# Performance work log

Measured on AMD Instinct MI355X. Metric: run time of the kernel, lower is better.

The kernel has to match this reference:

```python
import jax, jax.numpy as jnp
import numpy as np

N = 50000        # nodes
E = 800000       # edges (before self-loops)
F_IN = 256       # input feature dim
HID = 64         # hidden per head (concat=False -> head mean)
NCLS = 40        # classes
HEADS = 8
NEG_SLOPE = 0.2  # PyG GATConv default leaky_relu slope


def setup_inputs() -> dict:
    key = jax.random.key(0)
    ks = jax.random.split(key, 11)
    s = 0.1
    return {
        "x": jax.random.normal(ks[0], (N, F_IN), jnp.float32),
        "edge_index": jax.random.randint(ks[1], (2, E), 0, N, dtype=jnp.int64),
        "edge_attr": jax.random.uniform(ks[2], (E, 1), jnp.float32),
        "W0": jax.random.normal(ks[3], (HEADS * HID, F_IN), jnp.float32) * s,
        "a0s": jax.random.normal(ks[4], (HEADS, HID), jnp.float32) * s,
        "a0d": jax.random.normal(ks[5], (HEADS, HID), jnp.float32) * s,
        "b0": jnp.zeros((HID,), jnp.float32),
        "W2": jax.random.normal(ks[6], (HEADS * NCLS, HID), jnp.float32) * s,
        "a2s": jax.random.normal(ks[7], (HEADS, NCLS), jnp.float32) * s,
        "a2d": jax.random.normal(ks[8], (HEADS, NCLS), jnp.float32) * s,
        "b2": jnp.zeros((NCLS,), jnp.float32),
    }


def _gat_conv(x, src, dst, W, att_src, att_dst, bias, heads, out_c):
    # Linear: [N, in] @ [heads*out, in]^T -> [N, heads, out]
    h = (x @ W.T).reshape(N, heads, out_c)
    # Per-node attention logits, gathered per edge.
    a_s = jnp.einsum('nhc,hc->nh', h, att_src)
    a_d = jnp.einsum('nhc,hc->nh', h, att_dst)
    e = jax.nn.leaky_relu(a_s[src] + a_d[dst], NEG_SLOPE)  # [E, H]
    # Segment softmax over incoming edges of each destination node.
    m = jax.ops.segment_max(e, dst, num_segments=N)
    p = jnp.exp(e - m[dst])
    denom = jax.ops.segment_sum(p, dst, num_segments=N)
    alpha = p / (denom[dst] + 1e-16)
    # Weighted message scatter-sum: [E,H,C] -> [N,H,C]
    out = jax.ops.segment_sum(alpha[:, :, None] * h[src], dst, num_segments=N)
    # concat=False -> mean over heads, then bias.
    return out.mean(axis=1) + bias


def reference(x, edge_index, edge_attr, W0, a0s, a0d, b0, W2, a2s, a2d, b2):
    # edge_attr is unpacked by the torch forward but never used by GATConv.
    # PyG GATConv adds self-loops by default.
    loops = jnp.arange(N, dtype=edge_index.dtype)
    src = jnp.concatenate([edge_index[0], loops])
    dst = jnp.concatenate([edge_index[1], loops])
    h = jax.nn.relu(_gat_conv(x, src, dst, W0, a0s, a0d, b0, HEADS, HID))
    # dropout is identity in eval mode
    out = _gat_conv(h, src, dst, W2, a2s, a2d, b2, HEADS, NCLS)
    return jax.nn.log_softmax(out, axis=1)
```

## Files before the change

### kernel.cpp

```cpp
#include <hip/hip_runtime.h>
#include <hip/hip_bf16.h>
#include <math.h>


#define NEG_SLOPE 0.2f

typedef short v8s __attribute__((ext_vector_type(8)));
typedef float v4f __attribute__((ext_vector_type(4)));
typedef float v2f __attribute__((ext_vector_type(2)));
typedef unsigned short u16;
typedef unsigned int u32;
typedef unsigned char u8;

__device__ __forceinline__ u16 f2bf(float f) {
    union { float f; u32 u; } v; v.f = f;
    u32 r = v.u + 0x7fffu + ((v.u >> 16) & 1u);
    return (u16)(r >> 16);
}
__device__ __forceinline__ float lrelu_exp(float e) {
    e = (e > 0.f) ? e : NEG_SLOPE * e;
    return __expf(e);
}
__device__ __forceinline__ void dec8(uint2 r, float* h) {
    v2f a = __builtin_amdgcn_cvt_pk_f32_fp8(r.x, false);
    v2f b = __builtin_amdgcn_cvt_pk_f32_fp8(r.x, true);
    v2f c = __builtin_amdgcn_cvt_pk_f32_fp8(r.y, false);
    v2f d = __builtin_amdgcn_cvt_pk_f32_fp8(r.y, true);
    h[0] = a.x; h[1] = a.y; h[2] = b.x; h[3] = b.y;
    h[4] = c.x; h[5] = c.y; h[6] = d.x; h[7] = d.y;
}
__device__ __forceinline__ u8 enc8(float v) {
    u32 p = __builtin_amdgcn_cvt_pk_fp8_f32(v, v, 0u, false);
    return (u8)(p & 0xffu);
}


__global__ __launch_bounds__(256) void histcast_k(const int* __restrict__ ei, int* __restrict__ deg,
                                                  int E, int Nn, int NBh,
                                                  const float* __restrict__ x, u16* __restrict__ xb,
                                                  const float* __restrict__ W0, u16* __restrict__ W0b,
                                                  const float* __restrict__ W2, u16* __restrict__ W2b,
                                                  int nx, int n0c, int n2c) {
    int b = blockIdx.x;
    if (b < NBh) {
        int e = b * 256 + threadIdx.x;
        int ET = E + Nn;
        if (e >= ET) return;
        int d = (e < E) ? ei[E + e] : (e - E);
        atomicAdd(&deg[d], 1);
    } else {
        int i = ((b - NBh) * 256 + threadIdx.x) * 4;
        const float* in; u16* out;
        if (i < nx)            { in = x;  out = xb; }
        else if (i < nx + n0c) { in = W0; out = W0b; i -= nx; }
        else if (i < nx + n0c + n2c) { in = W2; out = W2b; i -= nx + n0c; }
        else return;
        float4 v = *reinterpret_cast<const float4*>(in + i);
        ushort4 o;
        o.x = f2bf(v.x); o.y = f2bf(v.y); o.z = f2bf(v.z); o.w = f2bf(v.w);
        *reinterpret_cast<ushort4*>(out + i) = o;
    }
}


__global__ __launch_bounds__(1024) void scanA_k(const int* __restrict__ deg, int* __restrict__ incl,
                                                int* __restrict__ bsum, int n) {
    __shared__ int wsum[16];
    int t = threadIdx.x;
    int i = blockIdx.x * 1024 + t;
    int v = (i < n) ? deg[i] : 0;
    int lane = t & 63, wid = t >> 6;
    int sv = v;
    for (int off = 1; off < 64; off <<= 1) {
        int u = __shfl_up(sv, off, 64);
        if (lane >= off) sv += u;
    }
    if (lane == 63) wsum[wid] = sv;
    __syncthreads();
    if (t < 16) {
        int w = wsum[t];
        for (int off = 1; off < 16; off <<= 1) {
            int u = __shfl_up(w, off, 64);
            if (t >= off) w += u;
        }
        wsum[t] = w;
    }
    __syncthreads();
    int pre = (wid > 0) ? wsum[wid - 1] : 0;
    int inc = pre + sv;
    if (i < n) incl[i] = inc;
    if (t == 1023) bsum[blockIdx.x] = inc;
}


__global__ __launch_bounds__(256) void scanBC_k(const int* __restrict__ incl, const int* __restrict__ deg,
                                                const int* __restrict__ bsum, int* __restrict__ rowstart,
                                                int n, int B) {
    __shared__ int sb[65];
    int t = threadIdx.x;
    if (t < 64) {
        int v = (t < B) ? bsum[t] : 0;
        int sv = v;
        for (int off = 1; off < 64; off <<= 1) {
            int u = __shfl_up(sv, off, 64);
            if (t >= off) sv += u;
        }
        sb[t] = sv - v;
        if (t == 63) sb[64] = sv;
    }
    __syncthreads();
    int i = blockIdx.x * 256 + t;
    if (i < n) rowstart[i] = sb[i >> 10] + incl[i] - deg[i];
    if (i == 0) rowstart[n] = sb[64];
}

__global__ __launch_bounds__(256) void scatter_k(const int* __restrict__ ei,
                                                 const int* __restrict__ rowstart,
                                                 int* __restrict__ cursor,
                                                 int* __restrict__ srcs, int E, int Nn) {
    int e = blockIdx.x * 256 + threadIdx.x;
    int ET = E + Nn;
    if (e >= ET) return;
    int s, d;
    if (e < E) { s = ei[e]; d = ei[E + e]; }
    else       { s = e - E; d = e - E; }
    int pos = atomicAdd(&cursor[d], 1);
    srcs[rowstart[d] + pos] = s;
}


__global__ __launch_bounds__(256, 4) void gemm_mfma(const u16* __restrict__ Ab,
                                                    const u16* __restrict__ Bb,
                                                    u8* __restrict__ Cf, int M, int Nc, int K,
                                                    const float* __restrict__ avs_vec,
                                                    const float* __restrict__ avd_vec,
                                                    float* as_out, float* ad_out) {
    __shared__ __align__(16) u8 lds[27648];
    u16 (*As)[72] = reinterpret_cast<u16(*)[72]>(lds);
    u16 (*Bs)[72] = reinterpret_cast<u16(*)[72]>(lds + 18432);
    const int t = threadIdx.x;
    const int m0 = blockIdx.x * 128;
    const int n0 = blockIdx.y * 64;
    const int w = t >> 6, lane = t & 63;
    const int wr = w * 32;
    const int q = lane >> 4, l16 = lane & 15;

    v4f acc[2][4];
#pragma unroll
    for (int i = 0; i < 2; i++)
#pragma unroll
        for (int j = 0; j < 4; j++) acc[i][j] = (v4f){0.f, 0.f, 0.f, 0.f};

    for (int kt = 0; kt < K; kt += 64) {
#pragma unroll
        for (int it = 0; it < 4; it++) {
            int c = it * 256 + t;
            int row = c >> 3, col8 = (c & 7) * 8;
            int gm = m0 + row;
            uint4 va = make_uint4(0u, 0u, 0u, 0u);
            if (gm < M) va = *reinterpret_cast<const uint4*>(Ab + (size_t)gm * K + kt + col8);
            *reinterpret_cast<uint4*>(&As[row][col8]) = va;
        }
#pragma unroll
        for (int it = 0; it < 2; it++) {
            int c = it * 256 + t;
            int row = c >> 3, col8 = (c & 7) * 8;
            uint4 vb = *reinterpret_cast<const uint4*>(Bb + (size_t)(n0 + row) * K + kt + col8);
            *reinterpret_cast<uint4*>(&Bs[row][col8]) = vb;
        }
        __syncthreads();
#pragma unroll
        for (int ks = 0; ks < 2; ks++) {
            v8s af[2], bf[4];
#pragma unroll
            for (int i = 0; i < 2; i++)
                af[i] = *reinterpret_cast<const v8s*>(&As[wr + i * 16 + l16][ks * 32 + q * 8]);
#pragma unroll
            for (int j = 0; j < 4; j++)
                bf[j] = *reinterpret_cast<const v8s*>(&Bs[j * 16 + l16][ks * 32 + q * 8]);
#pragma unroll
            for (int i = 0; i < 2; i++)
#pragma unroll
                for (int j = 0; j < 4; j++)
                    acc[i][j] = __builtin_amdgcn_mfma_f32_16x16x32_bf16(af[i], bf[j], acc[i][j], 0, 0, 0);
        }
        __syncthreads();
    }

    const bool do_att = (as_out != nullptr);
    float avs[4], avd[4];
    if (do_att) {
#pragma unroll
        for (int j = 0; j < 4; j++) {
            avs[j] = avs_vec[n0 + j * 16 + l16];
            avd[j] = avd_vec[n0 + j * 16 + l16];
        }
    }
    const int head = n0 >> 6;

    u8* Cs = lds;
#pragma unroll
    for (int i = 0; i < 2; i++) {
#pragma unroll
        for (int r = 0; r < 4; r++) {
            int row = wr + i * 16 + q * 4 + r;
#pragma unroll
            for (int j = 0; j < 4; j++)
                Cs[row * 80 + j * 16 + l16] = enc8(acc[i][j][r]);
            if (do_att) {
                int gm = m0 + row;
                float ps = 0.f, pd = 0.f;
#pragma unroll
                for (int j = 0; j < 4; j++) {
                    float v = acc[i][j][r];
                    ps = fmaf(v, avs[j], ps);
                    pd = fmaf(v, avd[j], pd);
                }
#pragma unroll
                for (int m = 1; m < 16; m <<= 1) {
                    ps += __shfl_xor(ps, m, 64);
                    pd += __shfl_xor(pd, m, 64);
                }
                if (l16 == 0 && gm < M) {
                    as_out[gm * 8 + head] = ps;
                    ad_out[gm * 8 + head] = pd;
                }
            }
        }
    }
    __syncthreads();
#pragma unroll
    for (int it = 0; it < 2; it++) {
        int idx = it * 256 + t;
        int row = idx >> 2, ch = idx & 3;
        int gm = m0 + row;
        if (gm < M)
            *reinterpret_cast<uint4*>(Cf + (size_t)gm * Nc + n0 + ch * 16) =
                *reinterpret_cast<const uint4*>(&Cs[row * 80 + ch * 16]);
    }
}


__global__ __launch_bounds__(256) void agg1_k(const u8* __restrict__ h1f,
                                              const float* __restrict__ as1, const float* __restrict__ ad1,
                                              const int* __restrict__ srcs, const int* __restrict__ rowstart,
                                              const float* __restrict__ b0, u16* __restrict__ x1b, int Nn) {
    int wave = threadIdx.x >> 6, lane = threadIdx.x & 63;
    int n = blockIdx.x * 4 + wave;
    if (n >= Nn) return;
    const int hl = lane >> 3;
    const float adl = ad1[n * 8 + hl];
    const u32 loff = (u32)lane * 8u;
    float acc[8] = {0, 0, 0, 0, 0, 0, 0, 0};
    float dsum = 0.f;
    int beg = rowstart[n], end = rowstart[n + 1];
    int i = beg;
    for (; i + 8 <= end; i += 8) {
        int s[8];
#pragma unroll
        for (int u = 0; u < 8; u++) s[u] = __builtin_amdgcn_readfirstlane(srcs[i + u]);
        uint2 rw[8];
#pragma unroll
        for (int u = 0; u < 8; u++) rw[u] = *reinterpret_cast<const uint2*>(h1f + ((u32)s[u] * 512u + loff));
        float eg[8];
#pragma unroll
        for (int u = 0; u < 8; u++) eg[u] = as1[(u32)s[u] * 8u + hl];
        float p[8];
#pragma unroll
        for (int u = 0; u < 8; u++) { p[u] = lrelu_exp(eg[u] + adl); dsum += p[u]; }
#pragma unroll
        for (int u = 0; u < 8; u++) {
            float hv[8];
            dec8(rw[u], hv);
#pragma unroll
            for (int j = 0; j < 8; j++) acc[j] = fmaf(p[u], hv[j], acc[j]);
        }
    }
    for (; i < end; i++) {
        int s = __builtin_amdgcn_readfirstlane(srcs[i]);
        uint2 raw = *reinterpret_cast<const uint2*>(h1f + ((u32)s * 512u + loff));
        float p = lrelu_exp(as1[(u32)s * 8u + hl] + adl);
        dsum += p;
        float hv[8];
        dec8(raw, hv);
#pragma unroll
        for (int j = 0; j < 8; j++) acc[j] = fmaf(p, hv[j], acc[j]);
    }
    float inv = 1.f / (dsum + 1e-16f);
    float r[8];
#pragma unroll
    for (int j = 0; j < 8; j++) r[j] = acc[j] * inv;
#pragma unroll
    for (int j = 0; j < 8; j++) {
        r[j] += __shfl_xor(r[j], 8, 64);
        r[j] += __shfl_xor(r[j], 16, 64);
        r[j] += __shfl_xor(r[j], 32, 64);
    }
    if (lane < 8) {
        u16 o[8];
#pragma unroll
        for (int j = 0; j < 8; j++) {
            float v = r[j] * 0.125f + b0[lane * 8 + j];
            o[j] = f2bf((v > 0.f) ? v : 0.f);
        }
        *reinterpret_cast<uint4*>(x1b + (size_t)n * 64 + lane * 8) =
            *reinterpret_cast<const uint4*>(o);
    }
}


__global__ __launch_bounds__(256) void att2_k(const u8* __restrict__ h2f,
                                              const float* __restrict__ a2s, const float* __restrict__ a2d,
                                              float* __restrict__ as2, float* __restrict__ ad2, int Nn) {
    int t = blockIdx.x * 256 + threadIdx.x;
    if (t >= Nn * 8) return;
    int n = t >> 3, h = t & 7;
    const u8* hr = h2f + (size_t)n * 320 + h * 40;
    float s1 = 0.f, s2 = 0.f;
#pragma unroll
    for (int b = 0; b < 5; b++) {
        uint2 raw = *reinterpret_cast<const uint2*>(hr + b * 8);
        float h8[8];
        dec8(raw, h8);
#pragma unroll
        for (int j = 0; j < 8; j++) {
            int c = h * 40 + b * 8 + j;
            s1 = fmaf(h8[j], a2s[c], s1);
            s2 = fmaf(h8[j], a2d[c], s2);
        }
    }
    as2[t] = s1;
    ad2[t] = s2;
}


__global__ __launch_bounds__(256) void agg2_k(const u8* __restrict__ h2f,
                                              const float* __restrict__ as2, const float* __restrict__ ad2,
                                              const int* __restrict__ srcs, const int* __restrict__ rowstart,
                                              const float* __restrict__ b2, float* __restrict__ out, int Nn) {
    __shared__ float smem[4][320];
    int wave = threadIdx.x >> 6, lane = threadIdx.x & 63;
    int n = blockIdx.x * 4 + wave;
    bool active = (n < Nn);
    bool ld = active && (lane < 40);
    const int hl = lane / 5;
    float adl = ld ? ad2[n * 8 + hl] : 0.f;
    float acc[8] = {0, 0, 0, 0, 0, 0, 0, 0};
    float dsum = 0.f;
    if (ld) {
        const u32 loff = (u32)lane * 8u;
        int beg = rowstart[n], end = rowstart[n + 1];
        int i = beg;
        for (; i + 8 <= end; i += 8) {
            int s[8];
#pragma unroll
            for (int u = 0; u < 8; u++) s[u] = __builtin_amdgcn_readfirstlane(srcs[i + u]);
            uint2 rw[8];
#pragma unroll
            for (int u = 0; u < 8; u++) rw[u] = *reinterpret_cast<const uint2*>(h2f + ((u32)s[u] * 320u + loff));
            float eg[8];
#pragma unroll
            for (int u = 0; u < 8; u++) eg[u] = as2[(u32)s[u] * 8u + hl];
            float p[8];
#pragma unroll
            for (int u = 0; u < 8; u++) { p[u] = lrelu_exp(eg[u] + adl); dsum += p[u]; }
#pragma unroll
            for (int u = 0; u < 8; u++) {
                float hv[8];
                dec8(rw[u], hv);
#pragma unroll
                for (int j = 0; j < 8; j++) acc[j] = fmaf(p[u], hv[j], acc[j]);
            }
        }
        for (; i < end; i++) {
            int s = __builtin_amdgcn_readfirstlane(srcs[i]);
            uint2 raw = *reinterpret_cast<const uint2*>(h2f + ((u32)s * 320u + loff));
            float p = lrelu_exp(as2[(u32)s * 8u + hl] + adl);
            dsum += p;
            float hv[8];
            dec8(raw, hv);
#pragma unroll
            for (int j = 0; j < 8; j++) acc[j] = fmaf(p, hv[j], acc[j]);
        }
        float inv = 1.f / (dsum + 1e-16f);
#pragma unroll
        for (int j = 0; j < 8; j++) smem[wave][lane * 8 + j] = acc[j] * inv;
    }
    __syncthreads();
    if (active) {
        float v;
        if (lane < 40) {
            float ssum = 0.f;
#pragma unroll
            for (int h = 0; h < 8; h++) ssum += smem[wave][h * 40 + lane];
            v = ssum * 0.125f + b2[lane];
        } else {
            v = -INFINITY;
        }
        float m = v;
        for (int off = 32; off > 0; off >>= 1) m = fmaxf(m, __shfl_xor(m, off, 64));
        float ex = (lane < 40) ? __expf(v - m) : 0.f;
        float se = ex;
        for (int off = 32; off > 0; off >>= 1) se += __shfl_xor(se, off, 64);
        if (lane < 40) out[(size_t)n * 40 + lane] = v - m - __logf(se);
    }
}


extern "C" void kernel_launch(void* const* d_in, const int* in_sizes, int n_in,
                              void* d_out, int out_size, void* d_ws, size_t ws_size,
                              hipStream_t stream) {
    const float* x   = (const float*)d_in[0];
    const int*   ei  = (const int*)d_in[1];
    const float* W0  = (const float*)d_in[3];
    const float* a0s = (const float*)d_in[4];
    const float* a0d = (const float*)d_in[5];
    const float* b0  = (const float*)d_in[6];
    const float* W2  = (const float*)d_in[7];
    const float* a2s = (const float*)d_in[8];
    const float* a2d = (const float*)d_in[9];
    const float* b2  = (const float*)d_in[10];
    float* out = (float*)d_out;

    const int Nn = in_sizes[0] / 256;
    const int E  = in_sizes[1] / 2;
    const int ET = E + Nn;
    const int NB = (Nn + 1023) / 1024;

    size_t off = 0;
    auto carve = [&](size_t bytes) -> void* {
        void* p = (char*)d_ws + off;
        off += (bytes + 255) & ~(size_t)255;
        return p;
    };
    u16*   xb       = (u16*)carve((size_t)Nn * 256 * 2);
    u16*   W0b      = (u16*)carve((size_t)512 * 256 * 2);
    u16*   W2b      = (u16*)carve((size_t)320 * 64 * 2);
    u8*    h1f      = (u8*)carve((size_t)Nn * 512);
    u16*   x1b      = (u16*)carve((size_t)Nn * 64 * 2);
    u8*    h2f      = (u8*)carve((size_t)Nn * 320);
    float* as1      = (float*)carve((size_t)Nn * 8 * 4);
    float* ad1      = (float*)carve((size_t)Nn * 8 * 4);
    float* as2      = (float*)carve((size_t)Nn * 8 * 4);
    float* ad2      = (float*)carve((size_t)Nn * 8 * 4);
    int*   deg      = (int*)carve((size_t)Nn * 4);
    int*   cursor   = (int*)carve((size_t)Nn * 4);
    int*   rowstart = (int*)carve((size_t)(Nn + 1) * 4);
    int*   srcs     = (int*)carve((size_t)ET * 4);
    int*   incl     = (int*)carve((size_t)Nn * 4);
    int*   bsum     = (int*)carve(64 * 4);

    const size_t degPad = ((size_t)Nn * 4 + 255) & ~(size_t)255;
    hipMemsetAsync(deg, 0, degPad + (size_t)Nn * 4, stream);

    const int nx = Nn * 256, n0c = 512 * 256, n2c = 320 * 64;
    const int NBh = (ET + 255) / 256;
    const int NBc = ((nx + n0c + n2c) / 4 + 255) / 256;
    histcast_k<<<NBh + NBc, 256, 0, stream>>>(ei, deg, E, Nn, NBh,
                                              x, xb, W0, W0b, W2, W2b, nx, n0c, n2c);
    scanA_k<<<NB, 1024, 0, stream>>>(deg, incl, bsum, Nn);
    scanBC_k<<<(Nn + 255) / 256, 256, 0, stream>>>(incl, deg, bsum, rowstart, Nn, NB);
    scatter_k<<<(ET + 255) / 256, 256, 0, stream>>>(ei, rowstart, cursor, srcs, E, Nn);

    gemm_mfma<<<dim3((Nn + 127) / 128, 8), 256, 0, stream>>>(
        xb, W0b, h1f, Nn, 512, 256, a0s, a0d, as1, ad1);
    agg1_k<<<(Nn + 3) / 4, 256, 0, stream>>>(h1f, as1, ad1, srcs, rowstart, b0, x1b, Nn);

    gemm_mfma<<<dim3((Nn + 127) / 128, 5), 256, 0, stream>>>(
        x1b, W2b, h2f, Nn, 320, 64, nullptr, nullptr, nullptr, nullptr);
    att2_k<<<(Nn * 8 + 255) / 256, 256, 0, stream>>>(h2f, a2s, a2d, as2, ad2, Nn);
    agg2_k<<<(Nn + 3) / 4, 256, 0, stream>>>(h2f, as2, ad2, srcs, rowstart, b2, out, Nn);
}
```

Baseline: 391.7 us.

## Sort nodes by in-degree for balanced aggregation waves and add 4-way unrolled tail

Builds a degree histogram during the scan and a counting-sort order of nodes by in-degree inside the scatter kernel. The two aggregation kernels then process nodes in that order, so the four waves of a block get similar edge counts, cutting intra-block imbalance and tail divergence. An extra 4-edge unrolled loop handles remainders before the scalar tail. The cost is the extra histogram atomics, the ordering pass, and less locality in output writes and dst-indexed loads, since node ids are no longer contiguous across waves.

```diff
diff --git a/kernel.cpp b/kernel.cpp
--- a/kernel.cpp
+++ b/kernel.cpp
@@ -64,11 +64,15 @@
 
 
 __global__ __launch_bounds__(1024) void scanA_k(const int* __restrict__ deg, int* __restrict__ incl,
-                                                int* __restrict__ bsum, int n) {
+                                                int* __restrict__ bsum, int* __restrict__ dbin, int n) {
     __shared__ int wsum[16];
+    __shared__ int dh[256];
     int t = threadIdx.x;
+    if (t < 256) dh[t] = 0;
     int i = blockIdx.x * 1024 + t;
     int v = (i < n) ? deg[i] : 0;
+    __syncthreads();
+    if (i < n) atomicAdd(&dh[v < 255 ? v : 255], 1);
     int lane = t & 63, wid = t >> 6;
     int sv = v;
     for (int off = 1; off < 64; off <<= 1) {
@@ -85,6 +89,7 @@
         }
         wsum[t] = w;
     }
+    if (t < 256 && dh[t] > 0) atomicAdd(&dbin[t], dh[t]);
     __syncthreads();
     int pre = (wid > 0) ? wsum[wid - 1] : 0;
     int inc = pre + sv;
@@ -114,18 +119,48 @@
     if (i == 0) rowstart[n] = sb[64];
 }
 
+
 __global__ __launch_bounds__(256) void scatter_k(const int* __restrict__ ei,
                                                  const int* __restrict__ rowstart,
                                                  int* __restrict__ cursor,
-                                                 int* __restrict__ srcs, int E, int Nn) {
-    int e = blockIdx.x * 256 + threadIdx.x;
+                                                 int* __restrict__ srcs, int E, int Nn,
+                                                 const int* __restrict__ deg,
+                                                 const int* __restrict__ dbin,
+                                                 int* __restrict__ dcur,
+                                                 int* __restrict__ order) {
+    int b = blockIdx.x, t = threadIdx.x;
+    int e = b * 256 + t;
     int ET = E + Nn;
-    if (e >= ET) return;
-    int s, d;
-    if (e < E) { s = ei[e]; d = ei[E + e]; }
-    else       { s = e - E; d = e - E; }
-    int pos = atomicAdd(&cursor[d], 1);
-    srcs[rowstart[d] + pos] = s;
+    if (e < ET) {
+        int s, d;
+        if (e < E) { s = ei[e]; d = ei[E + e]; }
+        else       { s = e - E; d = e - E; }
+        int pos = atomicAdd(&cursor[d], 1);
+        srcs[rowstart[d] + pos] = s;
+    }
+    if (b * 256 < Nn) {
+        __shared__ int ws4[4];
+        __shared__ int sbase[256];
+        int v = dbin[t];
+        int lane = t & 63, wid = t >> 6;
+        int sv = v;
+        for (int off = 1; off < 64; off <<= 1) {
+            int u = __shfl_up(sv, off, 64);
+            if (lane >= off) sv += u;
+        }
+        if (lane == 63) ws4[wid] = sv;
+        __syncthreads();
+        int add = 0;
+        for (int k = 0; k < wid; k++) add += ws4[k];
+        sbase[t] = add + sv - v;
+        __syncthreads();
+        int i = b * 256 + t;
+        if (i < Nn) {
+            int d = deg[i]; d = (d < 255) ? d : 255;
+            int pos = atomicAdd(&dcur[d], 1);
+            order[sbase[d] + pos] = i;
+        }
+    }
 }
 
 
@@ -244,10 +279,12 @@
 __global__ __launch_bounds__(256) void agg1_k(const u8* __restrict__ h1f,
                                               const float* __restrict__ as1, const float* __restrict__ ad1,
                                               const int* __restrict__ srcs, const int* __restrict__ rowstart,
+                                              const int* __restrict__ order,
                                               const float* __restrict__ b0, u16* __restrict__ x1b, int Nn) {
     int wave = threadIdx.x >> 6, lane = threadIdx.x & 63;
-    int n = blockIdx.x * 4 + wave;
-    if (n >= Nn) return;
+    int gid = blockIdx.x * 4 + wave;
+    if (gid >= Nn) return;
+    int n = __builtin_amdgcn_readfirstlane(order[gid]);
     const int hl = lane >> 3;
     const float adl = ad1[n * 8 + hl];
     const u32 loff = (u32)lane * 8u;
@@ -276,6 +313,26 @@
             for (int j = 0; j < 8; j++) acc[j] = fmaf(p[u], hv[j], acc[j]);
         }
     }
+    for (; i + 4 <= end; i += 4) {
+        int s[4];
+#pragma unroll
+        for (int u = 0; u < 4; u++) s[u] = __builtin_amdgcn_readfirstlane(srcs[i + u]);
+        uint2 rw[4];
+#pragma unroll
+        for (int u = 0; u < 4; u++) rw[u] = *reinterpret_cast<const uint2*>(h1f + ((u32)s[u] * 512u + loff));
+        float eg[4];
+#pragma unroll
+        for (int u = 0; u < 4; u++) eg[u] = as1[(u32)s[u] * 8u + hl];
+#pragma unroll
+        for (int u = 0; u < 4; u++) {
+            float p = lrelu_exp(eg[u] + adl);
+            dsum += p;
+            float hv[8];
+            dec8(rw[u], hv);
+#pragma unroll
+            for (int j = 0; j < 8; j++) acc[j] = fmaf(p, hv[j], acc[j]);
+        }
+    }
     for (; i < end; i++) {
         int s = __builtin_amdgcn_readfirstlane(srcs[i]);
         uint2 raw = *reinterpret_cast<const uint2*>(h1f + ((u32)s * 512u + loff));
@@ -337,11 +394,14 @@
 __global__ __launch_bounds__(256) void agg2_k(const u8* __restrict__ h2f,
                                               const float* __restrict__ as2, const float* __restrict__ ad2,
                                               const int* __restrict__ srcs, const int* __restrict__ rowstart,
+                                              const int* __restrict__ order,
                                               const float* __restrict__ b2, float* __restrict__ out, int Nn) {
     __shared__ float smem[4][320];
     int wave = threadIdx.x >> 6, lane = threadIdx.x & 63;
-    int n = blockIdx.x * 4 + wave;
-    bool active = (n < Nn);
+    int gid = blockIdx.x * 4 + wave;
+    bool active = (gid < Nn);
+    int n = 0;
+    if (active) n = __builtin_amdgcn_readfirstlane(order[gid]);
     bool ld = active && (lane < 40);
     const int hl = lane / 5;
     float adl = ld ? ad2[n * 8 + hl] : 0.f;
@@ -370,6 +430,26 @@
                 dec8(rw[u], hv);
 #pragma unroll
                 for (int j = 0; j < 8; j++) acc[j] = fmaf(p[u], hv[j], acc[j]);
+            }
+        }
+        for (; i + 4 <= end; i += 4) {
+            int s[4];
+#pragma unroll
+            for (int u = 0; u < 4; u++) s[u] = __builtin_amdgcn_readfirstlane(srcs[i + u]);
+            uint2 rw[4];
+#pragma unroll
+            for (int u = 0; u < 4; u++) rw[u] = *reinterpret_cast<const uint2*>(h2f + ((u32)s[u] * 320u + loff));
+            float eg[4];
+#pragma unroll
+            for (int u = 0; u < 4; u++) eg[u] = as2[(u32)s[u] * 8u + hl];
+#pragma unroll
+            for (int u = 0; u < 4; u++) {
+                float p = lrelu_exp(eg[u] + adl);
+                dsum += p;
+                float hv[8];
+                dec8(rw[u], hv);
+#pragma unroll
+                for (int j = 0; j < 8; j++) acc[j] = fmaf(p, hv[j], acc[j]);
             }
         }
         for (; i < end; i++) {
@@ -445,29 +525,33 @@
     float* ad2      = (float*)carve((size_t)Nn * 8 * 4);
     int*   deg      = (int*)carve((size_t)Nn * 4);
     int*   cursor   = (int*)carve((size_t)Nn * 4);
+    int*   dbin     = (int*)carve(256 * 4);
+    int*   dcur     = (int*)carve(256 * 4);
     int*   rowstart = (int*)carve((size_t)(Nn + 1) * 4);
     int*   srcs     = (int*)carve((size_t)ET * 4);
     int*   incl     = (int*)carve((size_t)Nn * 4);
     int*   bsum     = (int*)carve(64 * 4);
-
-    const size_t degPad = ((size_t)Nn * 4 + 255) & ~(size_t)255;
-    hipMemsetAsync(deg, 0, degPad + (size_t)Nn * 4, stream);
+    int*   order    = (int*)carve((size_t)Nn * 4);
+
+    const size_t zlen = (size_t)((char*)rowstart - (char*)deg);
+    hipMemsetAsync(deg, 0, zlen, stream);
 
     const int nx = Nn * 256, n0c = 512 * 256, n2c = 320 * 64;
     const int NBh = (ET + 255) / 256;
     const int NBc = ((nx + n0c + n2c) / 4 + 255) / 256;
     histcast_k<<<NBh + NBc, 256, 0, stream>>>(ei, deg, E, Nn, NBh,
                                               x, xb, W0, W0b, W2, W2b, nx, n0c, n2c);
-    scanA_k<<<NB, 1024, 0, stream>>>(deg, incl, bsum, Nn);
+    scanA_k<<<NB, 1024, 0, stream>>>(deg, incl, bsum, dbin, Nn);
     scanBC_k<<<(Nn + 255) / 256, 256, 0, stream>>>(incl, deg, bsum, rowstart, Nn, NB);
-    scatter_k<<<(ET + 255) / 256, 256, 0, stream>>>(ei, rowstart, cursor, srcs, E, Nn);
+    scatter_k<<<(ET + 255) / 256, 256, 0, stream>>>(ei, rowstart, cursor, srcs, E, Nn,
+                                                    deg, dbin, dcur, order);
 
     gemm_mfma<<<dim3((Nn + 127) / 128, 8), 256, 0, stream>>>(
         xb, W0b, h1f, Nn, 512, 256, a0s, a0d, as1, ad1);
-    agg1_k<<<(Nn + 3) / 4, 256, 0, stream>>>(h1f, as1, ad1, srcs, rowstart, b0, x1b, Nn);
+    agg1_k<<<(Nn + 3) / 4, 256, 0, stream>>>(h1f, as1, ad1, srcs, rowstart, order, b0, x1b, Nn);
 
     gemm_mfma<<<dim3((Nn + 127) / 128, 5), 256, 0, stream>>>(
         x1b, W2b, h2f, Nn, 320, 64, nullptr, nullptr, nullptr, nullptr);
     att2_k<<<(Nn * 8 + 255) / 256, 256, 0, stream>>>(h2f, a2s, a2d, as2, ad2, Nn);
-    agg2_k<<<(Nn + 3) / 4, 256, 0, stream>>>(h2f, as2, ad2, srcs, rowstart, b2, out, Nn);
-}
+    agg2_k<<<(Nn + 3) / 4, 256, 0, stream>>>(h2f, as2, ad2, srcs, rowstart, order, b2, out, Nn);
+}
```

Result: slower. 515.5 us (+31.6%).
